# Kernel optimization log

Measured on AMD Instinct MI355X. Metric: run time of the kernel, lower is better.

The kernel has to match this reference:

```python
import jax, jax.numpy as jnp
import numpy as np

B, C, F = 8, 2048, 128


def setup_inputs() -> dict:
    key = jax.random.key(0)
    ks = jax.random.split(key, 13)
    features = jax.random.normal(ks[0], (B, C, F), dtype=jnp.float32)
    # sparse-ish boolean adjacency masks over operations
    pred_mask = jax.random.uniform(ks[1], (B, C, C)) < 0.05
    succ_mask = jax.random.uniform(ks[2], (B, C, C)) < 0.05
    same_type_mask = jax.random.uniform(ks[3], (B, C, C)) < 0.10

    def linear(k, fan_in, fan_out):
        kw, kb = jax.random.split(k)
        bound = 1.0 / np.sqrt(fan_in)
        W = jax.random.uniform(kw, (fan_in, fan_out), minval=-bound, maxval=bound, dtype=jnp.float32)
        b = jax.random.uniform(kb, (fan_out,), minval=-bound, maxval=bound, dtype=jnp.float32)
        return W, b

    W_enc, b_enc = linear(ks[4], F, 4 * F)
    W_space, b_space = linear(ks[5], 3 * F, F)
    W_same, b_same = linear(ks[6], 2 * F, F)
    W_mix, b_mix = linear(ks[7], 2 * F, F)
    return {
        "features": features,
        "pred_mask": pred_mask,
        "succ_mask": succ_mask,
        "same_type_mask": same_type_mask,
        "W_enc": W_enc, "b_enc": b_enc,
        "W_space": W_space, "b_space": b_space,
        "W_same": W_same, "b_same": b_same,
        "W_mix": W_mix, "b_mix": b_mix,
    }


def reference(features, pred_mask, succ_mask, same_type_mask,
              W_enc, b_enc, W_space, b_space, W_same, b_same, W_mix, b_mix):
    # encoder: [B,C,F] -> [B,C,4F], split into origin + 3 message features
    enc = features @ W_enc + b_enc
    origin, e_pred, e_succ, e_same = jnp.split(enc, 4, axis=-1)

    def masked_mean(mask, e):
        # original builds (B,C,C,F) broadcast product then sums over 'other';
        # mathematically this is mask @ e with a clamped-degree divisor.
        m = mask.astype(e.dtype)                         # [B,C,C]
        deg = jnp.maximum(m.sum(-1, keepdims=True), 1.0)  # [B,C,1]
        return jnp.einsum('bij,bjf->bif', m, e) / deg

    pred_f = masked_mean(pred_mask, e_pred)
    succ_f = masked_mean(succ_mask, e_succ)
    same_f = masked_mean(same_type_mask, e_same)

    space_mixed = jnp.concatenate([pred_f, origin, succ_f], axis=-1) @ W_space + b_space
    same_mixed = jnp.concatenate([origin, same_f], axis=-1) @ W_same + b_same
    return jnp.concatenate([space_mixed, same_mixed], axis=-1) @ W_mix + b_mix
```

## Files before the change

kernel.cpp:

```cpp
#include <hip/hip_runtime.h>
#include <stdint.h>

typedef unsigned int uint;
typedef unsigned short ushort;
typedef unsigned char uchar;
typedef __attribute__((ext_vector_type(8))) short bf16x8;
typedef __attribute__((ext_vector_type(4))) float f32x4;

__device__ __forceinline__ ushort f2bf(float f) {
  uint u = __builtin_bit_cast(uint, f);
  return (ushort)((u + 0x7FFFu + ((u >> 16) & 1u)) >> 16);
}

__device__ __forceinline__ uint nz4(uint x) {
  uint y = (x & 0x7F7F7F7Fu) + 0x7F7F7F7Fu;
  uint z = (y | x) & 0x80808080u;
  return ((z >> 7) & 1u) | ((z >> 14) & 2u) | ((z >> 21) & 4u) | ((z >> 28) & 8u);
}
__device__ __forceinline__ bf16x8 bits2bf(uint byte) {
  bf16x8 r;
#pragma unroll
  for (int e = 0; e < 8; ++e)
    r[e] = (short)(ushort)(((byte >> e) & 1u) ? 0x3F80u : 0u);
  return r;
}

__global__ __launch_bounds__(256) void k_detect(
    const uint4* __restrict__ m, int* __restrict__ esz_out) {
  __shared__ int s_ok;
  if (threadIdx.x == 0) s_ok = 1;
  __syncthreads();
  int ok = 1;
#pragma unroll
  for (int i = 0; i < 16; ++i) {
    uint4 v = m[i * 256 + threadIdx.x];
    if (!(v.x <= 1u || v.x == 0x3F800000u)) ok = 0;
    if (!(v.y <= 1u || v.y == 0x3F800000u)) ok = 0;
    if (!(v.z <= 1u || v.z == 0x3F800000u)) ok = 0;
    if (!(v.w <= 1u || v.w == 0x3F800000u)) ok = 0;
  }
  if (!ok) atomicAnd(&s_ok, 0);
  __syncthreads();
  if (threadIdx.x == 0) *esz_out = s_ok ? 4 : 1;
}

__global__ __launch_bounds__(256) void k_front(
    const void* __restrict__ mp, const void* __restrict__ ms,
    const void* __restrict__ mt, uchar* __restrict__ pk,
    float* __restrict__ invdeg, const int* __restrict__ esz_p,
    const float* __restrict__ We, const float* __restrict__ Ws,
    const float* __restrict__ Wm, const float* __restrict__ Wx,
    ushort* __restrict__ Te, ushort* __restrict__ Ts,
    ushort* __restrict__ Tm, ushort* __restrict__ Tx) {
  __shared__ __align__(16) char smem[65536];
  const int t = threadIdx.x;
  if (blockIdx.x >= 1536) {
    int i = (blockIdx.x - 1536) * 256 + t;
    if (i < 65536) { int n = i >> 7, k = i & 127; Te[i] = f2bf(We[k * 512 + n]); return; }
    i -= 65536;
    if (i < 49152) { int n = i / 384, k = i - n * 384; Ts[i] = f2bf(Ws[k * 128 + n]); return; }
    i -= 49152;
    if (i < 32768) { int n = i >> 8, k = i & 255; Tm[i] = f2bf(Wm[k * 128 + n]); return; }
    i -= 32768;
    if (i < 32768) { int n = i >> 8, k = i & 255; Tx[i] = f2bf(Wx[k * 128 + n]); return; }
    return;
  }
  const int esz = *esz_p;
  const int lane = t & 63, wave = t >> 6;
  if (esz == 4) {
    const int wgid = blockIdx.x * 4 + wave;
    char* myl = smem + wave * 8192;

#define ROWPTR(RR)                                                            \
  ((const uchar*)((const uint*)((((RR) >> 14) == 0)   ? mp                    \
                                : (((RR) >> 14) == 1) ? ms                    \
                                                      : mt) +                 \
                  ((size_t)(((RR) >> 11) & 7) * 2048 + ((RR) & 2047)) * 2048))

#define ISSUE(RR, BUF)                                                        \
  {                                                                           \
    const uchar* gsrc_ = ROWPTR(RR);                                          \
    _Pragma("unroll") for (int ii = 0; ii < 8; ++ii)                          \
        __builtin_amdgcn_global_load_lds(                                     \
            (const __attribute__((address_space(1))) uint*)(gsrc_ +           \
                ii * 1024 + lane * 16),                                       \
            (__attribute__((address_space(3))) uint*)(myl + (BUF) * 32768 +   \
                ii * 1024 + lane * 16),                                       \
            16, 0, 0);                                                        \
  }

    ISSUE(wgid, 0)
    for (int r = 0; r < 8; ++r) {
      const int rr = wgid + r * 6144;
      if (r < 7) {
        ISSUE(rr + 6144, (r + 1) & 1)
        asm volatile("s_waitcnt vmcnt(8)" ::: "memory");
      } else {
        asm volatile("s_waitcnt vmcnt(0)" ::: "memory");
      }
      __builtin_amdgcn_sched_barrier(0);
      const char* rowl = myl + (r & 1) * 32768;
      unsigned long long kept = 0ull;
#pragma unroll
      for (int s = 0; s < 32; ++s) {
        uint v = *(const uint*)(rowl + s * 256 + lane * 4);
        unsigned long long bal = __ballot(v != 0u);
        if (lane == s) kept = bal;
      }
      int cnt = __popcll(kept);
#pragma unroll
      for (int o = 1; o < 64; o <<= 1) cnt += __shfl_xor(cnt, o);
      const int mid = rr >> 14, b = (rr >> 11) & 7, rrow = rr & 2047;
      const int mtile = rrow >> 6, rowin = rrow & 63;
      uchar* tb = pk + ((((size_t)(mid * 8 + b)) * 32 + mtile)) * 16384;
      if (lane < 32) {
        uint2 kv;
        kv.x = (uint)kept;
        kv.y = (uint)(kept >> 32);
        *(uint2*)(tb + rowin * 256 + ((lane ^ (rowin & 31)) << 3)) = kv;
      }
      if (lane == 0)
        invdeg[((size_t)mid * 8 + b) * 2048 + rrow] =
            1.0f / (float)(cnt > 0 ? cnt : 1);
    }
#undef ISSUE
#undef ROWPTR
  } else {
    const int gtid = blockIdx.x * 256 + t;
    for (int k = 0; k < 4; ++k) {
      const int u = gtid + k * 393216;
      const int row = u >> 5, seg = u & 31;
      const int mid = row >> 14, b = (row >> 11) & 7, rrow = row & 2047;
      const void* mask = (mid == 0) ? mp : (mid == 1) ? ms : mt;
      const uint4* p = (const uint4*)((const uchar*)mask +
                                      ((size_t)b * 2048 + rrow) * 2048 + seg * 64);
      uint4 v0 = p[0], v1 = p[1], v2 = p[2], v3 = p[3];
      uint q0 = nz4(v0.x) | (nz4(v0.y) << 4) | (nz4(v0.z) << 8) | (nz4(v0.w) << 12);
      uint q1 = nz4(v1.x) | (nz4(v1.y) << 4) | (nz4(v1.z) << 8) | (nz4(v1.w) << 12);
      uint q2 = nz4(v2.x) | (nz4(v2.y) << 4) | (nz4(v2.z) << 8) | (nz4(v2.w) << 12);
      uint q3 = nz4(v3.x) | (nz4(v3.y) << 4) | (nz4(v3.z) << 8) | (nz4(v3.w) << 12);
      uint lo = q0 | (q1 << 16);
      uint hi = q2 | (q3 << 16);
      int cnt = __popc(lo) + __popc(hi);
#pragma unroll
      for (int o = 1; o < 32; o <<= 1) cnt += __shfl_xor(cnt, o);
      if (seg == 0)
        invdeg[((size_t)mid * 8 + b) * 2048 + rrow] =
            1.0f / (float)(cnt > 0 ? cnt : 1);
      const int mtile = rrow >> 6, rowin = rrow & 63;
      uint2 w2v; w2v.x = lo; w2v.y = hi;
      *(uint2*)(pk + ((((size_t)(mid * 8 + b)) * 32 + mtile)) * 16384 +
                rowin * 256 + ((seg ^ (rowin & 31)) << 3)) = w2v;
    }
  }
}

__global__ __launch_bounds__(256) void k_enc(
    const float* __restrict__ features, const ushort* __restrict__ WTe,
    const float* __restrict__ bias, ushort* __restrict__ origin,
    ushort* __restrict__ eTt0, ushort* __restrict__ eTt1, ushort* __restrict__ eTt2) {
  __shared__ ushort tr[128 * 64];
  const int t = threadIdx.x;
  const int gm0 = blockIdx.x * 64;
  const int y = blockIdx.y;
  const int lane = t & 63, wave = t >> 6;
  const int m0w = (wave >> 1) * 32, n0w = (wave & 1) * 64;
  const int quad = lane >> 4, lr = lane & 15;
  const float* a0f = features + (size_t)(gm0 + m0w + lr) * 128 + quad * 8;
  const float* a1f = a0f + 16 * 128;
  bf16x8 af0[4], af1[4];
#pragma unroll
  for (int kc = 0; kc < 4; ++kc) {
    float4 x0 = *(const float4*)(a0f + kc * 32);
    float4 x1 = *(const float4*)(a0f + kc * 32 + 4);
    float4 y0 = *(const float4*)(a1f + kc * 32);
    float4 y1 = *(const float4*)(a1f + kc * 32 + 4);
    bf16x8 a, b;
    a[0] = (short)f2bf(x0.x); a[1] = (short)f2bf(x0.y);
    a[2] = (short)f2bf(x0.z); a[3] = (short)f2bf(x0.w);
    a[4] = (short)f2bf(x1.x); a[5] = (short)f2bf(x1.y);
    a[6] = (short)f2bf(x1.z); a[7] = (short)f2bf(x1.w);
    b[0] = (short)f2bf(y0.x); b[1] = (short)f2bf(y0.y);
    b[2] = (short)f2bf(y0.z); b[3] = (short)f2bf(y0.w);
    b[4] = (short)f2bf(y1.x); b[5] = (short)f2bf(y1.y);
    b[6] = (short)f2bf(y1.z); b[7] = (short)f2bf(y1.w);
    af0[kc] = a; af1[kc] = b;
  }
  f32x4 acc[2][4] = {};
#pragma unroll
  for (int j = 0; j < 4; ++j) {
    const ushort* bp = WTe + (size_t)(y * 128 + n0w + j * 16 + lr) * 128 + quad * 8;
#pragma unroll
    for (int kc = 0; kc < 4; ++kc) {
      bf16x8 bv = *(const bf16x8*)(bp + kc * 32);
      acc[0][j] = __builtin_amdgcn_mfma_f32_16x16x32_bf16(af0[kc], bv, acc[0][j], 0, 0, 0);
      acc[1][j] = __builtin_amdgcn_mfma_f32_16x16x32_bf16(af1[kc], bv, acc[1][j], 0, 0, 0);
    }
  }
  if (y == 0) {
#pragma unroll
    for (int i = 0; i < 2; ++i)
#pragma unroll
      for (int j = 0; j < 4; ++j) {
        int n = n0w + j * 16 + lr;
        float bb = bias[n];
        int mb = gm0 + m0w + i * 16 + quad * 4;
#pragma unroll
        for (int r = 0; r < 4; ++r)
          origin[(size_t)(mb + r) * 128 + n] = f2bf(acc[i][j][r] + bb);
      }
  } else {
#pragma unroll
    for (int i = 0; i < 2; ++i)
#pragma unroll
      for (int j = 0; j < 4; ++j) {
        int n = n0w + j * 16 + lr;
        float bb = bias[y * 128 + n];
        int m_lo = m0w + i * 16 + quad * 4;
        int chunk = m_lo >> 3;
        int byteo = n * 128 + ((chunk ^ (n & 7)) << 4) + (m_lo & 7) * 2;
        ushort4 o;
        o.x = f2bf(acc[i][j][0] + bb);
        o.y = f2bf(acc[i][j][1] + bb);
        o.z = f2bf(acc[i][j][2] + bb);
        o.w = f2bf(acc[i][j][3] + bb);
        *(ushort4*)((char*)tr + byteo) = o;
      }
    __syncthreads();
    ushort* eT = (y == 1) ? eTt0 : (y == 2) ? eTt1 : eTt2;
    const int bb_ = blockIdx.x >> 5, kstep = blockIdx.x & 31;
    uint4* dst = (uint4*)(eT + ((size_t)(bb_ * 32 + kstep)) * 8192);
    const uint4* src = (const uint4*)tr;
#pragma unroll
    for (int ii = 0; ii < 4; ++ii) dst[ii * 256 + t] = src[ii * 256 + t];
  }
}

__global__ __launch_bounds__(256, 3) void k_mm(
    const uchar* __restrict__ pk, const float* __restrict__ invdeg,
    const ushort* __restrict__ B0p, const ushort* __restrict__ B1p,
    const ushort* __restrict__ B2p,
    ushort* __restrict__ P, ushort* __restrict__ S, ushort* __restrict__ T) {
  __shared__ __align__(16) char smem[49152];
  const int t = threadIdx.x;
  const int g = blockIdx.x;
  const int X = g & 7, seq = g >> 3;
  const int pl = seq >> 5, mtile = seq & 31;
  const int panel = pl * 8 + X;
  const int b = panel / 3, mid = panel - b * 3;
  const ushort* Bt = (mid == 0) ? B0p : (mid == 1) ? B1p : B2p;
  ushort* outp = (mid == 0) ? P : (mid == 1) ? S : T;
  const uchar* pkT = pk + ((((size_t)(mid * 8 + b)) * 32 + mtile)) * 16384;
  const uchar* BtT = (const uchar*)Bt + ((size_t)b * 32) * 16384;
  const int lane = t & 63, wave = t >> 6;
  const int m0w = (wave >> 1) * 32, n0w = (wave & 1) * 64;
  const int quad = lane >> 4, lr = lane & 15;
  f32x4 acc[2][4] = {};

#define STG_A()                                                               \
  {                                                                           \
    _Pragma("unroll") for (int ii = 0; ii < 4; ++ii)                          \
        __builtin_amdgcn_global_load_lds(                                     \
            (const __attribute__((address_space(1))) uint*)(pkT +             \
                wave * 4096 + ii * 1024 + lane * 16),                         \
            (__attribute__((address_space(3))) uint*)(smem + wave * 4096 +    \
                ii * 1024 + lane * 16),                                       \
            16, 0, 0);                                                        \
  }
#define STG_B(BUF, STEP)                                                      \
  {                                                                           \
    _Pragma("unroll") for (int ii = 0; ii < 4; ++ii)                          \
        __builtin_amdgcn_global_load_lds(                                     \
            (const __attribute__((address_space(1))) uint*)(BtT +             \
                (size_t)(STEP) * 16384 + wave * 4096 + ii * 1024 + lane * 16),\
            (__attribute__((address_space(3))) uint*)(smem + 16384 +          \
                (BUF) * 16384 + wave * 4096 + ii * 1024 + lane * 16),         \
            16, 0, 0);                                                        \
  }
#define CPT(SS, BUF)                                                          \
  {                                                                           \
    const char* Ab = smem;                                                    \
    const char* Bb = smem + 16384 + (BUF) * 16384;                            \
    uint2 wa = *(const uint2*)(Ab + (m0w + lr) * 256 + (((SS) ^ lr) << 3));   \
    uint2 wb = *(const uint2*)(Ab + (m0w + 16 + lr) * 256 +                   \
                               (((SS) ^ (16 + lr)) << 3));                    \
    _Pragma("unroll") for (int kc = 0; kc < 2; ++kc) {                        \
      uint wax = kc ? wa.y : wa.x;                                            \
      uint wbx = kc ? wb.y : wb.x;                                            \
      bf16x8 a0 = bits2bf((wax >> (quad * 8)) & 0xFFu);                       \
      bf16x8 a1 = bits2bf((wbx >> (quad * 8)) & 0xFFu);                       \
      const int sl = (((kc * 4 + quad) ^ (lr & 7)) << 4);                     \
      bf16x8 b0 = *(const bf16x8*)(Bb + (n0w + lr) * 128 + sl);               \
      bf16x8 b1 = *(const bf16x8*)(Bb + (n0w + 16 + lr) * 128 + sl);          \
      bf16x8 b2 = *(const bf16x8*)(Bb + (n0w + 32 + lr) * 128 + sl);          \
      bf16x8 b3 = *(const bf16x8*)(Bb + (n0w + 48 + lr) * 128 + sl);          \
      __builtin_amdgcn_s_setprio(1);                                          \
      acc[0][0] = __builtin_amdgcn_mfma_f32_16x16x32_bf16(a0, b0, acc[0][0], 0, 0, 0); \
      acc[1][0] = __builtin_amdgcn_mfma_f32_16x16x32_bf16(a1, b0, acc[1][0], 0, 0, 0); \
      acc[0][1] = __builtin_amdgcn_mfma_f32_16x16x32_bf16(a0, b1, acc[0][1], 0, 0, 0); \
      acc[1][1] = __builtin_amdgcn_mfma_f32_16x16x32_bf16(a1, b1, acc[1][1], 0, 0, 0); \
      acc[0][2] = __builtin_amdgcn_mfma_f32_16x16x32_bf16(a0, b2, acc[0][2], 0, 0, 0); \
      acc[1][2] = __builtin_amdgcn_mfma_f32_16x16x32_bf16(a1, b2, acc[1][2], 0, 0, 0); \
      acc[0][3] = __builtin_amdgcn_mfma_f32_16x16x32_bf16(a0, b3, acc[0][3], 0, 0, 0); \
      acc[1][3] = __builtin_amdgcn_mfma_f32_16x16x32_bf16(a1, b3, acc[1][3], 0, 0, 0); \
      __builtin_amdgcn_s_setprio(0);                                          \
    }                                                                         \
  }

  STG_A()
  STG_B(0, 0)
  STG_B(1, 1)
  for (int s = 0; s < 32; ++s) {
    if (s < 31) asm volatile("s_waitcnt vmcnt(4)" ::: "memory");
    else        asm volatile("s_waitcnt vmcnt(0)" ::: "memory");
    __builtin_amdgcn_s_barrier();
    __builtin_amdgcn_sched_barrier(0);
    CPT(s, s & 1)
    asm volatile("" ::: "memory");
    __builtin_amdgcn_s_barrier();
    if (s < 30) STG_B(s & 1, s + 2)
  }
  __builtin_amdgcn_sched_barrier(0);
#undef CPT
#undef STG_B
#undef STG_A

  const size_t rowbase = (size_t)b * 2048 + mtile * 64;
  const float* inv = invdeg + ((size_t)(mid * 8 + b)) * 2048 + mtile * 64;
#pragma unroll
  for (int i = 0; i < 2; ++i)
#pragma unroll
    for (int r = 0; r < 4; ++r) {
      int ml = m0w + i * 16 + quad * 4 + r;
      float iv = inv[ml];
#pragma unroll
      for (int j = 0; j < 4; ++j) {
        int n = n0w + j * 16 + lr;
        outp[(rowbase + ml) * 128 + n] = f2bf(acc[i][j][r] * iv);
      }
    }
}

__device__ __forceinline__ void gemm_body(
    const ushort* __restrict__ A0, const ushort* __restrict__ A1,
    const ushort* __restrict__ A2, const ushort* __restrict__ Bsrc,
    int bstride, int K, const float* __restrict__ bias,
    void* __restrict__ out, int out_f32, int gm0, int t) {
  const int lane = t & 63, wave = t >> 6;
  const int m0w = (wave >> 1) * 32, n0w = (wave & 1) * 64;
  const int quad = lane >> 4, lr = lane & 15;
  const ushort* bbase = Bsrc + (size_t)(n0w + lr) * bstride + quad * 8;
  f32x4 acc[2][4] = {};
  for (int k0 = 0; k0 < K; k0 += 64) {
    const int seg = k0 >> 7;
    const ushort* Ap = (seg == 0) ? A0 : (seg == 1) ? A1 : A2;
    const int ko = k0 & 127;
    const ushort* a0p = Ap + (size_t)(gm0 + m0w + lr) * 128 + ko + quad * 8;
    const ushort* a1p = a0p + 16 * 128;
#pragma unroll
    for (int kc = 0; kc < 2; ++kc) {
      bf16x8 av0 = *(const bf16x8*)(a0p + kc * 32);
      bf16x8 av1 = *(const bf16x8*)(a1p + kc * 32);
      bf16x8 b0 = *(const bf16x8*)(bbase + k0 + kc * 32);
      bf16x8 b1 = *(const bf16x8*)(bbase + (size_t)16 * bstride + k0 + kc * 32);
      bf16x8 b2 = *(const bf16x8*)(bbase + (size_t)32 * bstride + k0 + kc * 32);
      bf16x8 b3 = *(const bf16x8*)(bbase + (size_t)48 * bstride + k0 + kc * 32);
      acc[0][0] = __builtin_amdgcn_mfma_f32_16x16x32_bf16(av0, b0, acc[0][0], 0, 0, 0);
      acc[1][0] = __builtin_amdgcn_mfma_f32_16x16x32_bf16(av1, b0, acc[1][0], 0, 0, 0);
      acc[0][1] = __builtin_amdgcn_mfma_f32_16x16x32_bf16(av0, b1, acc[0][1], 0, 0, 0);
      acc[1][1] = __builtin_amdgcn_mfma_f32_16x16x32_bf16(av1, b1, acc[1][1], 0, 0, 0);
      acc[0][2] = __builtin_amdgcn_mfma_f32_16x16x32_bf16(av0, b2, acc[0][2], 0, 0, 0);
      acc[1][2] = __builtin_amdgcn_mfma_f32_16x16x32_bf16(av1, b2, acc[1][2], 0, 0, 0);
      acc[0][3] = __builtin_amdgcn_mfma_f32_16x16x32_bf16(av0, b3, acc[0][3], 0, 0, 0);
      acc[1][3] = __builtin_amdgcn_mfma_f32_16x16x32_bf16(av1, b3, acc[1][3], 0, 0, 0);
    }
  }
#pragma unroll
  for (int i = 0; i < 2; ++i)
#pragma unroll
    for (int j = 0; j < 4; ++j) {
      const int n = n0w + j * 16 + lr;
      const float bb = bias[n];
      const int mb = gm0 + m0w + i * 16 + quad * 4;
      if (out_f32) {
#pragma unroll
        for (int r = 0; r < 4; ++r)
          ((float*)out)[(size_t)(mb + r) * 128 + n] = acc[i][j][r] + bb;
      } else {
#pragma unroll
        for (int r = 0; r < 4; ++r)
          ((ushort*)out)[(size_t)(mb + r) * 128 + n] = f2bf(acc[i][j][r] + bb);
      }
    }
}

__global__ __launch_bounds__(256) void k_xy(
    const ushort* __restrict__ P, const ushort* __restrict__ origin,
    const ushort* __restrict__ S, const ushort* __restrict__ T,
    const ushort* __restrict__ WTs, const ushort* __restrict__ WTm,
    const float* __restrict__ bs, const float* __restrict__ bm,
    ushort* __restrict__ X, ushort* __restrict__ Y) {
  const int gm0 = blockIdx.x * 64;
  if (blockIdx.y == 0)
    gemm_body(P, origin, S, WTs, 384, 384, bs, X, 0, gm0, threadIdx.x);
  else
    gemm_body(origin, T, nullptr, WTm, 256, 256, bm, Y, 0, gm0, threadIdx.x);
}

__global__ __launch_bounds__(256) void k_mix(
    const ushort* __restrict__ X, const ushort* __restrict__ Y,
    const ushort* __restrict__ WTx, const float* __restrict__ bx,
    float* __restrict__ out) {
  gemm_body(X, Y, nullptr, WTx, 256, 256, bx, out, 1, blockIdx.x * 64, threadIdx.x);
}

extern "C" void kernel_launch(void* const* d_in, const int* in_sizes, int n_in,
                              void* d_out, int out_size, void* d_ws,
                              size_t ws_size, hipStream_t stream) {
  const float* features = (const float*)d_in[0];
  const void* pred = d_in[1];
  const void* succ = d_in[2];
  const void* same = d_in[3];
  const float* W_enc = (const float*)d_in[4];
  const float* b_enc = (const float*)d_in[5];
  const float* W_space = (const float*)d_in[6];
  const float* b_space = (const float*)d_in[7];
  const float* W_same = (const float*)d_in[8];
  const float* b_same = (const float*)d_in[9];
  const float* W_mix = (const float*)d_in[10];
  const float* b_mix = (const float*)d_in[11];

  const size_t M = 16384;
  ushort* w = (ushort*)d_ws;
  ushort* WT_enc = w;   w += 512 * 128;
  ushort* WT_space = w; w += 128 * 384;
  ushort* WT_same = w;  w += 128 * 256;
  ushort* WT_mix = w;   w += 128 * 256;
  ushort* origin = w;   w += M * 128;
  ushort* eTt0 = w;     w += M * 128;
  ushort* eTt1 = w;     w += M * 128;
  ushort* eTt2 = w;     w += M * 128;
  ushort* P = w;        w += M * 128;
  ushort* S = w;        w += M * 128;
  ushort* T = w;        w += M * 128;
  uchar* pk = (uchar*)w;
  ushort* X = w;
  ushort* Y = w + M * 128;
  w += 6291456;
  float* invdeg = (float*)w;  w += 98304;
  int* esz = (int*)w;

  k_detect<<<1, 256, 0, stream>>>((const uint4*)pred, esz);
  k_front<<<2240, 256, 0, stream>>>(pred, succ, same, pk, invdeg, esz,
                                    W_enc, W_space, W_same, W_mix,
                                    WT_enc, WT_space, WT_same, WT_mix);
  k_enc<<<dim3(256, 4), 256, 0, stream>>>(features, WT_enc, b_enc,
                                          origin, eTt0, eTt1, eTt2);
  k_mm<<<768, 256, 0, stream>>>(pk, invdeg, eTt0, eTt1, eTt2, P, S, T);
  k_xy<<<dim3(256, 2), 256, 0, stream>>>(P, origin, S, T, WT_space, WT_same,
                                         b_space, b_same, X, Y);
  k_mix<<<256, 256, 0, stream>>>(X, Y, WT_mix, b_mix, (float*)d_out);
}
```

Baseline: 474.6 us.

## Inline mask dtype detection per block and split front kernel into halves

Removes the single-block detect kernel and has each k_front block re-check the first 16KB of the pred mask itself. The weight transpose moves into its own kernel, and the mask-packing work is split across two launches of 768 blocks covering half the rows each. This drops one serial tiny launch from the critical path, at the cost of redundant detection reads in every block and an extra launch.

```diff
diff --git a/kernel.cpp b/kernel.cpp
--- a/kernel.cpp
+++ b/kernel.cpp
@@ -25,47 +25,47 @@
   return r;
 }
 
-__global__ __launch_bounds__(256) void k_detect(
-    const uint4* __restrict__ m, int* __restrict__ esz_out) {
-  __shared__ int s_ok;
-  if (threadIdx.x == 0) s_ok = 1;
-  __syncthreads();
+__device__ __forceinline__ int detect_esz_block(const uint4* m, char* smem) {
   int ok = 1;
-#pragma unroll
-  for (int i = 0; i < 16; ++i) {
-    uint4 v = m[i * 256 + threadIdx.x];
+  for (int i = threadIdx.x; i < 1024; i += 256) {
+    uint4 v = m[i];
     if (!(v.x <= 1u || v.x == 0x3F800000u)) ok = 0;
     if (!(v.y <= 1u || v.y == 0x3F800000u)) ok = 0;
     if (!(v.z <= 1u || v.z == 0x3F800000u)) ok = 0;
     if (!(v.w <= 1u || v.w == 0x3F800000u)) ok = 0;
   }
-  if (!ok) atomicAnd(&s_ok, 0);
+  int* flag = (int*)smem;
+  if (threadIdx.x == 0) *flag = 1;
   __syncthreads();
-  if (threadIdx.x == 0) *esz_out = s_ok ? 4 : 1;
-}
-
-__global__ __launch_bounds__(256) void k_front(
-    const void* __restrict__ mp, const void* __restrict__ ms,
-    const void* __restrict__ mt, uchar* __restrict__ pk,
-    float* __restrict__ invdeg, const int* __restrict__ esz_p,
+  if (!ok) *flag = 0;
+  __syncthreads();
+  int esz = *flag ? 4 : 1;
+  __syncthreads();
+  return esz;
+}
+
+__global__ __launch_bounds__(256) void k_wt(
     const float* __restrict__ We, const float* __restrict__ Ws,
     const float* __restrict__ Wm, const float* __restrict__ Wx,
     ushort* __restrict__ Te, ushort* __restrict__ Ts,
     ushort* __restrict__ Tm, ushort* __restrict__ Tx) {
+  int i = blockIdx.x * 256 + threadIdx.x;
+  if (i < 65536) { int n = i >> 7, k = i & 127; Te[i] = f2bf(We[k * 512 + n]); return; }
+  i -= 65536;
+  if (i < 49152) { int n = i / 384, k = i - n * 384; Ts[i] = f2bf(Ws[k * 128 + n]); return; }
+  i -= 49152;
+  if (i < 32768) { int n = i >> 8, k = i & 255; Tm[i] = f2bf(Wm[k * 128 + n]); return; }
+  i -= 32768;
+  if (i < 32768) { int n = i >> 8, k = i & 255; Tx[i] = f2bf(Wx[k * 128 + n]); return; }
+}
+
+__global__ __launch_bounds__(256) void k_front(
+    const void* __restrict__ mp, const void* __restrict__ ms,
+    const void* __restrict__ mt, uchar* __restrict__ pk,
+    float* __restrict__ invdeg, int row0) {
   __shared__ __align__(16) char smem[65536];
   const int t = threadIdx.x;
-  if (blockIdx.x >= 1536) {
-    int i = (blockIdx.x - 1536) * 256 + t;
-    if (i < 65536) { int n = i >> 7, k = i & 127; Te[i] = f2bf(We[k * 512 + n]); return; }
-    i -= 65536;
-    if (i < 49152) { int n = i / 384, k = i - n * 384; Ts[i] = f2bf(Ws[k * 128 + n]); return; }
-    i -= 49152;
-    if (i < 32768) { int n = i >> 8, k = i & 255; Tm[i] = f2bf(Wm[k * 128 + n]); return; }
-    i -= 32768;
-    if (i < 32768) { int n = i >> 8, k = i & 255; Tx[i] = f2bf(Wx[k * 128 + n]); return; }
-    return;
-  }
-  const int esz = *esz_p;
+  const int esz = detect_esz_block((const uint4*)mp, smem);
   const int lane = t & 63, wave = t >> 6;
   if (esz == 4) {
     const int wgid = blockIdx.x * 4 + wave;
@@ -89,11 +89,11 @@
             16, 0, 0);                                                        \
   }
 
-    ISSUE(wgid, 0)
+    ISSUE(row0 + wgid, 0)
     for (int r = 0; r < 8; ++r) {
-      const int rr = wgid + r * 6144;
+      const int rr = row0 + wgid + r * 3072;
       if (r < 7) {
-        ISSUE(rr + 6144, (r + 1) & 1)
+        ISSUE(rr + 3072, (r + 1) & 1)
         asm volatile("s_waitcnt vmcnt(8)" ::: "memory");
       } else {
         asm volatile("s_waitcnt vmcnt(0)" ::: "memory");
@@ -127,8 +127,9 @@
 #undef ROWPTR
   } else {
     const int gtid = blockIdx.x * 256 + t;
+    const int u0 = row0 * 32;
     for (int k = 0; k < 4; ++k) {
-      const int u = gtid + k * 393216;
+      const int u = u0 + gtid + k * 196608;
       const int row = u >> 5, seg = u & 31;
       const int mid = row >> 14, b = (row >> 11) & 7, rrow = row & 2047;
       const void* mask = (mid == 0) ? mp : (mid == 1) ? ms : mt;
@@ -448,12 +449,11 @@
   ushort* Y = w + M * 128;
   w += 6291456;
   float* invdeg = (float*)w;  w += 98304;
-  int* esz = (int*)w;
-
-  k_detect<<<1, 256, 0, stream>>>((const uint4*)pred, esz);
-  k_front<<<2240, 256, 0, stream>>>(pred, succ, same, pk, invdeg, esz,
-                                    W_enc, W_space, W_same, W_mix,
-                                    WT_enc, WT_space, WT_same, WT_mix);
+
+  k_wt<<<704, 256, 0, stream>>>(W_enc, W_space, W_same, W_mix,
+                                WT_enc, WT_space, WT_same, WT_mix);
+  k_front<<<768, 256, 0, stream>>>(pred, succ, same, pk, invdeg, 0);
+  k_front<<<768, 256, 0, stream>>>(pred, succ, same, pk, invdeg, 24576);
   k_enc<<<dim3(256, 4), 256, 0, stream>>>(features, WT_enc, b_enc,
                                           origin, eTt0, eTt1, eTt2);
   k_mm<<<768, 256, 0, stream>>>(pk, invdeg, eTt0, eTt1, eTt2, P, S, T);
```

Result: no change. 479.9 us (+1.1%).
